# Kernel optimization log

Measured on AMD Instinct MI355X. Metric: run time of the kernel, lower is better.

The kernel has to match this reference:

```python
import jax, jax.numpy as jnp
import numpy as np

SQ3 = np.float32(np.sqrt(3.0))
NS, NV = 8, 4  # irreps 8x0e + 4x1o (dim 20)
N_NODES, N_EDGES = 10000, 160000


def _mlp(x, W1, W2):
    # e3nn FullyConnectedNet: act between layers, weights scaled by 1/sqrt(fan_in)
    h = jax.nn.relu(x @ (W1 / np.float32(np.sqrt(W1.shape[0]))))
    return h @ (W2 / np.float32(np.sqrt(W2.shape[0])))


def _tp(s, v, sh1, w_ss, w_vs, w_sv, w_vv):
    # FullyConnectedTensorProduct with per-edge weights, lmax=1 sh (sh0 == 1).
    # s:[E,Ms] scalars, v:[E,Mv,3] vectors, sh1:[E,3] component-normalized l=1 SH.
    Ms, Mv = s.shape[1], v.shape[1]
    c_s = np.float32(1.0 / np.sqrt(2.0 * Ms))
    c_v = np.float32(1.0 / np.sqrt(2.0 * Mv))
    # 0e x 0e -> 0e  and  1o x 1o -> 0e (dot / sqrt(3))
    dots = jnp.einsum('eic,ec->ei', v, sh1) / SQ3
    out0 = jnp.einsum('ei,eio->eo', s, w_ss) * c_s + jnp.einsum('ei,eio->eo', dots, w_vs) * c_v
    # 0e x 1o -> 1o  and  1o x 0e -> 1o
    out1 = jnp.einsum('ei,ec,eio->eoc', s, sh1, w_sv) * c_s + jnp.einsum('eic,eio->eoc', v, w_vv) * c_v
    return out0, out1


def setup_inputs() -> dict:
    key = jax.random.key(0)
    ks = jax.random.split(key, 16)
    N, E = N_NODES, N_EDGES
    return {
        'hn': jax.random.normal(ks[0], (N, 20), jnp.float32),
        'he': jax.random.normal(ks[1], (E, 20), jnp.float32),
        'edge_src': jax.random.randint(ks[2], (E,), 0, N),
        'edge_dst': jax.random.randint(ks[3], (E,), 0, N),
        'edge_vec': jax.random.normal(ks[4], (E, 3), jnp.float32),
        'emb': jax.random.uniform(ks[5], (E, 10), jnp.float32),
        'norm': jax.random.uniform(ks[6], (E,), jnp.float32),
        'num_nodes': N,
        'fcW1': jax.random.normal(ks[7], (10, 16), jnp.float32),
        'fcW2': jax.random.normal(ks[8], (16, 576), jnp.float32),
        'fc2W1': jax.random.normal(ks[9], (10, 16), jnp.float32),
        'fc2W2': jax.random.normal(ks[10], (16, 144), jnp.float32),
        'WgS': jax.random.normal(ks[11], (16, 12), jnp.float32),
        'WgV': jax.random.normal(ks[12], (8, 4), jnp.float32),
        'WoS': jax.random.normal(ks[13], (8, 8), jnp.float32),
        'WoV': jax.random.normal(ks[14], (4, 4), jnp.float32),
    }


def reference(hn, he, edge_src, edge_dst, edge_vec, emb, norm, num_nodes,
              fcW1, fcW2, fc2W1, fc2W2, WgS, WgV, WoS, WoV):
    E = he.shape[0]
    split = lambda x: (x[:, :NS], x[:, NS:].reshape(-1, NV, 3))
    hn_s, hn_v = split(hn)
    he_s, he_v = split(he)

    # spherical harmonics, normalize=True, component normalization, lmax=1
    sh1 = SQ3 * edge_vec / (jnp.linalg.norm(edge_vec, axis=1, keepdims=True) + 1e-12)

    s_in = jnp.concatenate([he_s, hn_s[edge_src], hn_s[edge_dst]], axis=1)       # [E,24]
    v_in = jnp.concatenate([he_v, hn_v[edge_src], hn_v[edge_dst]], axis=1)       # [E,12,3]

    # per-edge TP1 weights from tiny MLP on edge embedding (weight_numel = 576)
    w = _mlp(emb, fcW1, fcW2)
    w_ss = w[:, :288].reshape(E, 24, 12)
    w_vs = w[:, 288:432].reshape(E, 12, 12)
    w_sv = w[:, 432:528].reshape(E, 24, 4)
    w_vv = w[:, 528:576].reshape(E, 12, 4)
    g0, g1 = _tp(s_in, v_in, sh1, w_ss, w_vs, w_sv, w_vv)                        # [E,12],[E,4,3]

    # Gate: 8x0e scalars (ReLU), 4x0e gates (ReLU) gating 4x1o
    tmp_s = jax.nn.relu(g0[:, :NS])
    gates = jax.nn.relu(g0[:, NS:NS + NV])
    tmp_v = g1 * gates[:, :, None]

    # per-edge TP2 weights (weight_numel = 144)
    w2 = _mlp(emb, fc2W1, fc2W2)
    w2_ss = w2[:, :64].reshape(E, 8, 8)
    w2_vs = w2[:, 64:96].reshape(E, 4, 8)
    w2_sv = w2[:, 96:128].reshape(E, 8, 4)
    w2_vv = w2[:, 128:144].reshape(E, 4, 4)
    d0, d1 = _tp(tmp_s, tmp_v, sh1, w2_ss, w2_vs, w2_sv, w2_vv)

    he_new = jnp.concatenate([he_s + d0, (he_v + d1).reshape(E, NV * 3)], axis=1)

    # scatter-aggregate edge features to destination nodes
    node_ftr = jax.ops.segment_sum(he_new * norm[:, None], edge_dst, num_segments=num_nodes)
    nf_s, nf_v = node_ftr[:, :NS], node_ftr[:, NS:].reshape(-1, NV, 3)

    # lin = o3GatedLinear(input+output -> output) then o3.Linear(output -> output)
    cat_s = jnp.concatenate([hn_s, nf_s], axis=1)                                # [N,16]
    cat_v = jnp.concatenate([hn_v, nf_v], axis=1)                                # [N,8,3]
    g_lin = cat_s @ (WgS / np.float32(np.sqrt(16.0)))                            # [N,12]
    v_lin = jnp.einsum('nic,io->noc', cat_v, WgV) / np.float32(np.sqrt(8.0))     # [N,4,3]
    ls = jax.nn.relu(g_lin[:, :NS])
    lg = jax.nn.relu(g_lin[:, NS:])
    lv = v_lin * lg[:, :, None]
    out_s = ls @ (WoS / np.float32(np.sqrt(8.0)))
    out_v = jnp.einsum('nic,io->noc', lv, WoV) / np.float32(np.sqrt(4.0))

    hn_new = hn + jnp.concatenate([out_s, out_v.reshape(-1, NV * 3)], axis=1)
    return hn_new, he_new
```

## Files before the change

### kernel.cpp

```cpp
#include <hip/hip_runtime.h>

typedef __attribute__((ext_vector_type(8))) short bf16x8;
typedef __attribute__((ext_vector_type(4))) short bf16x4;
typedef __attribute__((ext_vector_type(4))) float f32x4;
typedef unsigned short ushort_t;

#define EPB 256
#define ST  32
#define W1S 632
#define W2S 168
#define HHS 40
#define TPS 40

__device__ __forceinline__ float frelu(float x) { return fmaxf(x, 0.0f); }

__device__ __forceinline__ ushort_t f2bf(float f) {
    unsigned u = __float_as_uint(f);
    u = (u + 0x7FFFu + ((u >> 16) & 1u)) >> 16;
    return (ushort_t)u;
}
__device__ __forceinline__ float bf2f(ushort_t u) {
    return __uint_as_float(((unsigned)u) << 16);
}

__device__ __forceinline__ float dot8(const float* s, bf16x8 w) {
    float a = 0.f;
#pragma unroll
    for (int b = 0; b < 8; ++b) a = fmaf(s[b], bf2f((ushort_t)w[b]), a);
    return a;
}
__device__ __forceinline__ float dot4(const float* s, bf16x4 w) {
    float a = 0.f;
#pragma unroll
    for (int b = 0; b < 4; ++b) a = fmaf(s[b], bf2f((ushort_t)w[b]), a);
    return a;
}

__global__ void prep_kernel(const float* __restrict__ fcW2,
                            const float* __restrict__ fc2W2,
                            ushort_t* __restrict__ W1t,
                            ushort_t* __restrict__ W2t) {
    const float SQ3 = 1.7320508075688772f;
    const float cs1 = 0.14433756729740643f;
    const float cv1 = 0.20412414523193150f;
    const float cs2 = 0.25f;
    const float cv2 = 0.35355339059327373f;
    int idx = blockIdx.x * blockDim.x + threadIdx.x;
    if (idx < 576 * 16) {
        int c = idx >> 4, k = idx & 15;
        float s = (c < 288) ? cs1 : (c < 432) ? cv1 : (c < 528) ? SQ3 * cs1 : cv1;
        W1t[idx] = f2bf(fcW2[k * 576 + c] * 0.25f * s);
    }
    if (idx < 144 * 16) {
        int c = idx >> 4, k = idx & 15;
        float s = (c < 64) ? cs2 : (c < 96) ? cv2 : (c < 128) ? SQ3 * cs2 : cv2;
        W2t[idx] = f2bf(fc2W2[k * 144 + c] * 0.25f * s);
    }
}

__global__ __launch_bounds__(EPB) void edge_kernel(
    const float* __restrict__ hn, const float* __restrict__ he,
    const int* __restrict__ esrc, const int* __restrict__ edst,
    const float* __restrict__ evec, const float* __restrict__ emb,
    const float* __restrict__ enorm,
    const float* __restrict__ fcW1, const float* __restrict__ fc2W1,
    const ushort_t* __restrict__ W1t, const ushort_t* __restrict__ W2t,
    float* __restrict__ he_out, float* __restrict__ node_ftr, int E) {

    __shared__ ushort_t hh[EPB][HHS];
    __shared__ ushort_t W1L[ST][W1S];
    __shared__ ushort_t W2L[ST][W2S];
    __shared__ ushort_t tmpL[ST][TPS];

    const int tid  = threadIdx.x;
    const int wave = tid >> 6;
    const int lane = tid & 63;
    const int row  = lane & 15;
    const int g    = lane >> 4;
    const long long blk = blockIdx.x;

    bf16x8 Bf[12];
#pragma unroll
    for (int idx = 0; idx < 12; ++idx) {
        int t = wave + idx * 4;
        bf16x8 v = {};
        if (t < 45 && g < 2) {
            const ushort_t* src = (t < 36) ? (W1t + (t * 16 + row) * 16 + g * 8)
                                           : (W2t + ((t - 36) * 16 + row) * 16 + g * 8);
            v = *reinterpret_cast<const bf16x8*>(src);
        }
        Bf[idx] = v;
    }

    {
        long long e0 = blk * EPB + tid;
        if (e0 < (long long)E) {
            float em[10];
#pragma unroll
            for (int i = 0; i < 10; ++i) em[i] = emb[e0 * 10 + i] * 0.31622776601683794f;
#pragma unroll
            for (int jj = 0; jj < 16; ++jj) {
                float a = 0.f, b = 0.f;
#pragma unroll
                for (int i = 0; i < 10; ++i) {
                    a = fmaf(em[i], fcW1[i * 16 + jj], a);
                    b = fmaf(em[i], fc2W1[i * 16 + jj], b);
                }
                hh[tid][jj]      = f2bf(frelu(a));
                hh[tid][16 + jj] = f2bf(frelu(b));
            }
        } else {
#pragma unroll
            for (int jj = 0; jj < 32; ++jj) hh[tid][jj] = 0;
        }
    }
    __syncthreads();

    const int le = tid & 31;
    const int j  = tid >> 5;

    for (int st = 0; st < 8; ++st) {
        long long ge = blk * EPB + st * ST + le;
        bool on = ge < (long long)E;

        int nd = 0;
        float ex = 0, ey = 0, ez = 0, nw = 0;
        float her[20], hsr[20], hdr[20];
        if (on) {
            int ns = esrc[ge];
            nd = edst[ge];
            ex = evec[ge * 3 + 0]; ey = evec[ge * 3 + 1]; ez = evec[ge * 3 + 2];
            nw = enorm[ge];
            const float* hp = he + ge * 20;
            const float* sp = hn + (long long)ns * 20;
            const float* dp = hn + (long long)nd * 20;
#pragma unroll
            for (int q = 0; q < 20; ++q) { her[q] = hp[q]; hsr[q] = sp[q]; hdr[q] = dp[q]; }
        } else {
#pragma unroll
            for (int q = 0; q < 20; ++q) { her[q] = 0; hsr[q] = 0; hdr[q] = 0; }
        }

        bf16x8 A1[2] = {}, A2[2] = {};
        if (g < 2) {
#pragma unroll
            for (int m = 0; m < 2; ++m) {
                A1[m] = *reinterpret_cast<const bf16x8*>(&hh[st * ST + m * 16 + row][g * 8]);
                A2[m] = *reinterpret_cast<const bf16x8*>(&hh[st * ST + m * 16 + row][16 + g * 8]);
            }
        }
#pragma unroll
        for (int idx = 0; idx < 12; ++idx) {
            int t = wave + idx * 4;
            if (t >= 45) continue;
            bool isg1 = (t < 36);
            int c = (isg1 ? t * 16 : (t - 36) * 16) + row;
            int off;
            if (isg1) {
                if (c < 288)      { int i = c / 12,          o = c % 12;         off = o * 24 + i; }
                else if (c < 432) { int i = (c - 288) / 12,  o = (c - 288) % 12; off = 288 + o * 12 + i; }
                else if (c < 528) { int i = (c - 432) >> 2,  o = (c - 432) & 3;  off = 432 + o * 24 + i; }
                else              { int i = (c - 528) >> 2,  o = (c - 528) & 3;  off = 528 + o * 12 + i; }
            } else {
                if (c < 64)       { int i = c >> 3,          o = c & 7;          off = o * 8 + i; }
                else if (c < 96)  { int i = (c - 64) >> 3,   o = (c - 64) & 7;   off = 64 + o * 4 + i; }
                else if (c < 128) { int i = (c - 96) >> 2,   o = (c - 96) & 3;   off = 96 + o * 8 + i; }
                else              { int i = (c - 128) >> 2,  o = (c - 128) & 3;  off = 128 + o * 4 + i; }
            }
            f32x4 zero = {0.f, 0.f, 0.f, 0.f};
#pragma unroll
            for (int m = 0; m < 2; ++m) {
                f32x4 d = __builtin_amdgcn_mfma_f32_16x16x32_bf16(isg1 ? A1[m] : A2[m], Bf[idx], zero, 0, 0, 0);
                int r0 = m * 16 + g * 4;
                if (isg1) {
#pragma unroll
                    for (int r = 0; r < 4; ++r) W1L[r0 + r][off] = f2bf(d[r]);
                } else {
#pragma unroll
                    for (int r = 0; r < 4; ++r) W2L[r0 + r][off] = f2bf(d[r]);
                }
            }
        }
        __syncthreads();

        float u0 = 0, u1 = 0, u2 = 0;
        if (on) {
            float inv = 1.0f / (sqrtf(fmaf(ex, ex, fmaf(ey, ey, ez * ez))) + 1e-12f);
            u0 = ex * inv; u1 = ey * inv; u2 = ez * inv;
            const ushort_t* base = &W1L[le][0];

            if (j < 6) {
                float dots[12];
#pragma unroll
                for (int i = 0; i < 4; ++i) {
                    dots[i]     = fmaf(her[8 + i * 3], u0, fmaf(her[9 + i * 3], u1, her[10 + i * 3] * u2));
                    dots[4 + i] = fmaf(hsr[8 + i * 3], u0, fmaf(hsr[9 + i * 3], u1, hsr[10 + i * 3] * u2));
                    dots[8 + i] = fmaf(hdr[8 + i * 3], u0, fmaf(hdr[9 + i * 3], u1, hdr[10 + i * 3] * u2));
                }
#pragma unroll
                for (int oo = 0; oo < 2; ++oo) {
                    int o = 2 * j + oo;
                    bf16x8 wa = *reinterpret_cast<const bf16x8*>(base + o * 24);
                    bf16x8 wb = *reinterpret_cast<const bf16x8*>(base + o * 24 + 8);
                    bf16x8 wc = *reinterpret_cast<const bf16x8*>(base + o * 24 + 16);
                    float acc = dot8(her, wa) + dot8(hsr, wb) + dot8(hdr, wc);
                    bf16x4 va = *reinterpret_cast<const bf16x4*>(base + 288 + o * 12);
                    bf16x4 vb = *reinterpret_cast<const bf16x4*>(base + 288 + o * 12 + 4);
                    bf16x4 vc = *reinterpret_cast<const bf16x4*>(base + 288 + o * 12 + 8);
                    acc += dot4(dots, va) + dot4(dots + 4, vb) + dot4(dots + 8, vc);
                    tmpL[le][o] = f2bf(acc);
                }
            } else {
#pragma unroll
                for (int oo = 0; oo < 2; ++oo) {
                    int o = 2 * (j - 6) + oo;
                    bf16x8 p0 = *reinterpret_cast<const bf16x8*>(base + 432 + o * 24);
                    bf16x8 p1 = *reinterpret_cast<const bf16x8*>(base + 432 + o * 24 + 8);
                    bf16x8 p2 = *reinterpret_cast<const bf16x8*>(base + 432 + o * 24 + 16);
                    float q = dot8(her, p0) + dot8(hsr, p1) + dot8(hdr, p2);
                    bf16x4 q0 = *reinterpret_cast<const bf16x4*>(base + 528 + o * 12);
                    bf16x4 q1 = *reinterpret_cast<const bf16x4*>(base + 528 + o * 12 + 4);
                    bf16x4 q2 = *reinterpret_cast<const bf16x4*>(base + 528 + o * 12 + 8);
                    float vx = 0, vy = 0, vz = 0;
#pragma unroll
                    for (int i = 0; i < 4; ++i) {
                        float w = bf2f((ushort_t)q0[i]);
                        vx = fmaf(her[8 + i * 3], w, vx); vy = fmaf(her[9 + i * 3], w, vy); vz = fmaf(her[10 + i * 3], w, vz);
                    }
#pragma unroll
                    for (int i = 0; i < 4; ++i) {
                        float w = bf2f((ushort_t)q1[i]);
                        vx = fmaf(hsr[8 + i * 3], w, vx); vy = fmaf(hsr[9 + i * 3], w, vy); vz = fmaf(hsr[10 + i * 3], w, vz);
                    }
#pragma unroll
                    for (int i = 0; i < 4; ++i) {
                        float w = bf2f((ushort_t)q2[i]);
                        vx = fmaf(hdr[8 + i * 3], w, vx); vy = fmaf(hdr[9 + i * 3], w, vy); vz = fmaf(hdr[10 + i * 3], w, vz);
                    }
                    tmpL[le][12 + 3 * o + 0] = f2bf(fmaf(q, u0, vx));
                    tmpL[le][12 + 3 * o + 1] = f2bf(fmaf(q, u1, vy));
                    tmpL[le][12 + 3 * o + 2] = f2bf(fmaf(q, u2, vz));
                }
            }
        }
        __syncthreads();

        if (on) {
            bf16x8 t0 = *reinterpret_cast<const bf16x8*>(&tmpL[le][0]);
            bf16x8 t1 = *reinterpret_cast<const bf16x8*>(&tmpL[le][8]);
            bf16x8 t2 = *reinterpret_cast<const bf16x8*>(&tmpL[le][16]);
            float ts[8];
#pragma unroll
            for (int b = 0; b < 8; ++b) ts[b] = frelu(bf2f((ushort_t)t0[b]));
            float gt[4];
#pragma unroll
            for (int o = 0; o < 4; ++o) gt[o] = frelu(bf2f((ushort_t)t1[o]));
            float tv[4][3];
#pragma unroll
            for (int o = 0; o < 4; ++o) {
#pragma unroll
                for (int c = 0; c < 3; ++c) {
                    int sl = 12 + 3 * o + c;
                    float raw = (sl < 16) ? bf2f((ushort_t)t1[sl - 8]) : bf2f((ushort_t)t2[sl - 16]);
                    tv[o][c] = raw * gt[o];
                }
            }
            float d2[4];
#pragma unroll
            for (int i = 0; i < 4; ++i) d2[i] = fmaf(tv[i][0], u0, fmaf(tv[i][1], u1, tv[i][2] * u2));

            const ushort_t* b2 = &W2L[le][0];
            float* hep = he_out + ge * 20;
            float* nf  = node_ftr + (long long)nd * 20;

            {
                bf16x8 wss = *reinterpret_cast<const bf16x8*>(b2 + j * 8);
                bf16x4 wvs = *reinterpret_cast<const bf16x4*>(b2 + 64 + j * 4);
                float dval = dot8(ts, wss) + dot4(d2, wvs);
                float oS = he[ge * 20 + j] + dval;
                hep[j] = oS;
                atomicAdd(nf + j, oS * nw);
            }
            if (j < 4) {
                bf16x8 wsv = *reinterpret_cast<const bf16x8*>(b2 + 96 + j * 8);
                float q2s = dot8(ts, wsv);
                bf16x4 wvv = *reinterpret_cast<const bf16x4*>(b2 + 128 + j * 4);
                float e0c = 0, e1c = 0, e2c = 0;
#pragma unroll
                for (int i = 0; i < 4; ++i) {
                    float w = bf2f((ushort_t)wvv[i]);
                    e0c = fmaf(tv[i][0], w, e0c); e1c = fmaf(tv[i][1], w, e1c); e2c = fmaf(tv[i][2], w, e2c);
                }
                float d1c[3] = { fmaf(q2s, u0, e0c), fmaf(q2s, u1, e1c), fmaf(q2s, u2, e2c) };
#pragma unroll
                for (int c = 0; c < 3; ++c) {
                    float oV = he[ge * 20 + 8 + 3 * j + c] + d1c[c];
                    hep[8 + 3 * j + c] = oV;
                    atomicAdd(nf + 8 + 3 * j + c, oV * nw);
                }
            }
        }
        __syncthreads();
    }
}

__global__ __launch_bounds__(256) void node_kernel(
    const float* __restrict__ hn, const float* __restrict__ node_ftr,
    const float* __restrict__ WgS, const float* __restrict__ WgV,
    const float* __restrict__ WoS, const float* __restrict__ WoV,
    float* __restrict__ out, int N) {
    int n = blockIdx.x * blockDim.x + threadIdx.x;
    if (n >= N) return;
    const float* hr = hn + (size_t)n * 20;
    const float* fr = node_ftr + (size_t)n * 20;
    const float rs16 = 0.25f, rs8 = 0.35355339059327373f, rs4 = 0.5f;

    float cs[16], cvx[8], cvy[8], cvz[8];
#pragma unroll
    for (int i = 0; i < 8; ++i) { cs[i] = hr[i]; cs[8 + i] = fr[i]; }
#pragma unroll
    for (int i = 0; i < 4; ++i) {
        cvx[i] = hr[8 + i * 3]; cvy[i] = hr[8 + i * 3 + 1]; cvz[i] = hr[8 + i * 3 + 2];
        cvx[4 + i] = fr[8 + i * 3]; cvy[4 + i] = fr[8 + i * 3 + 1]; cvz[4 + i] = fr[8 + i * 3 + 2];
    }
    float gl[12];
#pragma unroll
    for (int o = 0; o < 12; ++o) {
        float a = 0.f;
#pragma unroll
        for (int i = 0; i < 16; ++i) a = fmaf(cs[i], WgS[i * 12 + o], a);
        gl[o] = a * rs16;
    }
    float vlx[4], vly[4], vlz[4];
#pragma unroll
    for (int o = 0; o < 4; ++o) {
        float ax = 0.f, ay = 0.f, az = 0.f;
#pragma unroll
        for (int i = 0; i < 8; ++i) {
            float w = WgV[i * 4 + o];
            ax = fmaf(cvx[i], w, ax); ay = fmaf(cvy[i], w, ay); az = fmaf(cvz[i], w, az);
        }
        float gv = frelu(gl[8 + o]);
        vlx[o] = ax * rs8 * gv; vly[o] = ay * rs8 * gv; vlz[o] = az * rs8 * gv;
    }
    float ls[8];
#pragma unroll
    for (int i = 0; i < 8; ++i) ls[i] = frelu(gl[i]);
    float* op = out + (size_t)n * 20;
#pragma unroll
    for (int o = 0; o < 8; ++o) {
        float a = 0.f;
#pragma unroll
        for (int i = 0; i < 8; ++i) a = fmaf(ls[i], WoS[i * 8 + o], a);
        op[o] = hr[o] + a * rs8;
    }
#pragma unroll
    for (int o = 0; o < 4; ++o) {
        float ax = 0.f, ay = 0.f, az = 0.f;
#pragma unroll
        for (int i = 0; i < 4; ++i) {
            float w = WoV[i * 4 + o];
            ax = fmaf(vlx[i], w, ax); ay = fmaf(vly[i], w, ay); az = fmaf(vlz[i], w, az);
        }
        op[8 + o * 3 + 0] = hr[8 + o * 3 + 0] + ax * rs4;
        op[8 + o * 3 + 1] = hr[8 + o * 3 + 1] + ay * rs4;
        op[8 + o * 3 + 2] = hr[8 + o * 3 + 2] + az * rs4;
    }
}

extern "C" void kernel_launch(void* const* d_in, const int* in_sizes, int n_in,
                              void* d_out, int out_size, void* d_ws, size_t ws_size,
                              hipStream_t stream) {
    const float* hn    = (const float*)d_in[0];
    const float* he    = (const float*)d_in[1];
    const int*   esrc  = (const int*)d_in[2];
    const int*   edst  = (const int*)d_in[3];
    const float* evec  = (const float*)d_in[4];
    const float* emb   = (const float*)d_in[5];
    const float* enorm = (const float*)d_in[6];
    const float* fcW1  = (const float*)d_in[8];
    const float* fcW2  = (const float*)d_in[9];
    const float* fc2W1 = (const float*)d_in[10];
    const float* fc2W2 = (const float*)d_in[11];
    const float* WgS   = (const float*)d_in[12];
    const float* WgV   = (const float*)d_in[13];
    const float* WoS   = (const float*)d_in[14];
    const float* WoV   = (const float*)d_in[15];

    int N = in_sizes[0] / 20;
    int E = in_sizes[1] / 20;

    float* out      = (float*)d_out;
    float* he_out   = out + (size_t)N * 20;
    float* node_ftr = (float*)d_ws;
    ushort_t* W1t   = (ushort_t*)(node_ftr + (size_t)N * 20);
    ushort_t* W2t   = W1t + 576 * 16;

    hipMemsetAsync(node_ftr, 0, (size_t)N * 20 * sizeof(float), stream);
    prep_kernel<<<(576 * 16 + 255) / 256, 256, 0, stream>>>(fcW2, fc2W2, W1t, W2t);
    edge_kernel<<<(E + EPB - 1) / EPB, EPB, 0, stream>>>(
        hn, he, esrc, edst, evec, emb, enorm, fcW1, fc2W1, W1t, W2t, he_out, node_ftr, E);
    node_kernel<<<(N + 255) / 256, 256, 0, stream>>>(hn, node_ftr, WgS, WgV, WoS, WoV, out, N);
}
```

Baseline: 256.2 us.

## Halve edge sub-tile and spread per-edge outputs across more threads

Shrinks the per-iteration sub-tile from 32 to 16 edges, so each of the 256 threads computes one output channel instead of two, and the final stage splits scalar and vector outputs across separate thread groups. The goal is to cut serial work per thread and the shared weight tile footprint. In exchange there are twice as many loop iterations and block barriers, and each MFMA call covers half as many rows, so weight generation may use the matrix unit less efficiently. The node-feature memset is also folded into the prep kernel to drop one launch.

```diff
diff --git a/kernel.cpp b/kernel.cpp
--- a/kernel.cpp
+++ b/kernel.cpp
@@ -6,7 +6,7 @@
 typedef unsigned short ushort_t;
 
 #define EPB 256
-#define ST  32
+#define ST  16
 #define W1S 632
 #define W2S 168
 #define HHS 40
@@ -39,7 +39,8 @@
 __global__ void prep_kernel(const float* __restrict__ fcW2,
                             const float* __restrict__ fc2W2,
                             ushort_t* __restrict__ W1t,
-                            ushort_t* __restrict__ W2t) {
+                            ushort_t* __restrict__ W2t,
+                            float* __restrict__ node_ftr, int nfcount) {
     const float SQ3 = 1.7320508075688772f;
     const float cs1 = 0.14433756729740643f;
     const float cv1 = 0.20412414523193150f;
@@ -56,6 +57,7 @@
         float s = (c < 64) ? cs2 : (c < 96) ? cv2 : (c < 128) ? SQ3 * cs2 : cv2;
         W2t[idx] = f2bf(fc2W2[k * 144 + c] * 0.25f * s);
     }
+    if (idx < nfcount) node_ftr[idx] = 0.f;
 }
 
 __global__ __launch_bounds__(EPB) void edge_kernel(
@@ -116,10 +118,10 @@
     }
     __syncthreads();
 
-    const int le = tid & 31;
-    const int j  = tid >> 5;
-
-    for (int st = 0; st < 8; ++st) {
+    const int le = tid & 15;
+    const int j  = tid >> 4;
+
+    for (int st = 0; st < 16; ++st) {
         long long ge = blk * EPB + st * ST + le;
         bool on = ge < (long long)E;
 
@@ -141,13 +143,10 @@
             for (int q = 0; q < 20; ++q) { her[q] = 0; hsr[q] = 0; hdr[q] = 0; }
         }
 
-        bf16x8 A1[2] = {}, A2[2] = {};
+        bf16x8 A1 = {}, A2 = {};
         if (g < 2) {
-#pragma unroll
-            for (int m = 0; m < 2; ++m) {
-                A1[m] = *reinterpret_cast<const bf16x8*>(&hh[st * ST + m * 16 + row][g * 8]);
-                A2[m] = *reinterpret_cast<const bf16x8*>(&hh[st * ST + m * 16 + row][16 + g * 8]);
-            }
+            A1 = *reinterpret_cast<const bf16x8*>(&hh[st * ST + row][g * 8]);
+            A2 = *reinterpret_cast<const bf16x8*>(&hh[st * ST + row][16 + g * 8]);
         }
 #pragma unroll
         for (int idx = 0; idx < 12; ++idx) {
@@ -168,17 +167,14 @@
                 else              { int i = (c - 128) >> 2,  o = (c - 128) & 3;  off = 128 + o * 4 + i; }
             }
             f32x4 zero = {0.f, 0.f, 0.f, 0.f};
-#pragma unroll
-            for (int m = 0; m < 2; ++m) {
-                f32x4 d = __builtin_amdgcn_mfma_f32_16x16x32_bf16(isg1 ? A1[m] : A2[m], Bf[idx], zero, 0, 0, 0);
-                int r0 = m * 16 + g * 4;
-                if (isg1) {
-#pragma unroll
-                    for (int r = 0; r < 4; ++r) W1L[r0 + r][off] = f2bf(d[r]);
-                } else {
-#pragma unroll
-                    for (int r = 0; r < 4; ++r) W2L[r0 + r][off] = f2bf(d[r]);
-                }
+            f32x4 d = __builtin_amdgcn_mfma_f32_16x16x32_bf16(isg1 ? A1 : A2, Bf[idx], zero, 0, 0, 0);
+            int r0 = g * 4;
+            if (isg1) {
+#pragma unroll
+                for (int r = 0; r < 4; ++r) W1L[r0 + r][off] = f2bf(d[r]);
+            } else {
+#pragma unroll
+                for (int r = 0; r < 4; ++r) W2L[r0 + r][off] = f2bf(d[r]);
             }
         }
         __syncthreads();
@@ -189,7 +185,7 @@
             u0 = ex * inv; u1 = ey * inv; u2 = ez * inv;
             const ushort_t* base = &W1L[le][0];
 
-            if (j < 6) {
+            if (j < 12) {
                 float dots[12];
 #pragma unroll
                 for (int i = 0; i < 4; ++i) {
@@ -197,55 +193,49 @@
                     dots[4 + i] = fmaf(hsr[8 + i * 3], u0, fmaf(hsr[9 + i * 3], u1, hsr[10 + i * 3] * u2));
                     dots[8 + i] = fmaf(hdr[8 + i * 3], u0, fmaf(hdr[9 + i * 3], u1, hdr[10 + i * 3] * u2));
                 }
-#pragma unroll
-                for (int oo = 0; oo < 2; ++oo) {
-                    int o = 2 * j + oo;
-                    bf16x8 wa = *reinterpret_cast<const bf16x8*>(base + o * 24);
-                    bf16x8 wb = *reinterpret_cast<const bf16x8*>(base + o * 24 + 8);
-                    bf16x8 wc = *reinterpret_cast<const bf16x8*>(base + o * 24 + 16);
-                    float acc = dot8(her, wa) + dot8(hsr, wb) + dot8(hdr, wc);
-                    bf16x4 va = *reinterpret_cast<const bf16x4*>(base + 288 + o * 12);
-                    bf16x4 vb = *reinterpret_cast<const bf16x4*>(base + 288 + o * 12 + 4);
-                    bf16x4 vc = *reinterpret_cast<const bf16x4*>(base + 288 + o * 12 + 8);
-                    acc += dot4(dots, va) + dot4(dots + 4, vb) + dot4(dots + 8, vc);
-                    tmpL[le][o] = f2bf(acc);
-                }
+                int o = j;
+                bf16x8 wa = *reinterpret_cast<const bf16x8*>(base + o * 24);
+                bf16x8 wb = *reinterpret_cast<const bf16x8*>(base + o * 24 + 8);
+                bf16x8 wc = *reinterpret_cast<const bf16x8*>(base + o * 24 + 16);
+                float acc = dot8(her, wa) + dot8(hsr, wb) + dot8(hdr, wc);
+                bf16x4 va = *reinterpret_cast<const bf16x4*>(base + 288 + o * 12);
+                bf16x4 vb = *reinterpret_cast<const bf16x4*>(base + 288 + o * 12 + 4);
+                bf16x4 vc = *reinterpret_cast<const bf16x4*>(base + 288 + o * 12 + 8);
+                acc += dot4(dots, va) + dot4(dots + 4, vb) + dot4(dots + 8, vc);
+                tmpL[le][o] = f2bf(acc);
             } else {
-#pragma unroll
-                for (int oo = 0; oo < 2; ++oo) {
-                    int o = 2 * (j - 6) + oo;
-                    bf16x8 p0 = *reinterpret_cast<const bf16x8*>(base + 432 + o * 24);
-                    bf16x8 p1 = *reinterpret_cast<const bf16x8*>(base + 432 + o * 24 + 8);
-                    bf16x8 p2 = *reinterpret_cast<const bf16x8*>(base + 432 + o * 24 + 16);
-                    float q = dot8(her, p0) + dot8(hsr, p1) + dot8(hdr, p2);
-                    bf16x4 q0 = *reinterpret_cast<const bf16x4*>(base + 528 + o * 12);
-                    bf16x4 q1 = *reinterpret_cast<const bf16x4*>(base + 528 + o * 12 + 4);
-                    bf16x4 q2 = *reinterpret_cast<const bf16x4*>(base + 528 + o * 12 + 8);
-                    float vx = 0, vy = 0, vz = 0;
-#pragma unroll
-                    for (int i = 0; i < 4; ++i) {
-                        float w = bf2f((ushort_t)q0[i]);
-                        vx = fmaf(her[8 + i * 3], w, vx); vy = fmaf(her[9 + i * 3], w, vy); vz = fmaf(her[10 + i * 3], w, vz);
-                    }
-#pragma unroll
-                    for (int i = 0; i < 4; ++i) {
-                        float w = bf2f((ushort_t)q1[i]);
-                        vx = fmaf(hsr[8 + i * 3], w, vx); vy = fmaf(hsr[9 + i * 3], w, vy); vz = fmaf(hsr[10 + i * 3], w, vz);
-                    }
-#pragma unroll
-                    for (int i = 0; i < 4; ++i) {
-                        float w = bf2f((ushort_t)q2[i]);
-                        vx = fmaf(hdr[8 + i * 3], w, vx); vy = fmaf(hdr[9 + i * 3], w, vy); vz = fmaf(hdr[10 + i * 3], w, vz);
-                    }
-                    tmpL[le][12 + 3 * o + 0] = f2bf(fmaf(q, u0, vx));
-                    tmpL[le][12 + 3 * o + 1] = f2bf(fmaf(q, u1, vy));
-                    tmpL[le][12 + 3 * o + 2] = f2bf(fmaf(q, u2, vz));
-                }
+                int o = j - 12;
+                bf16x8 p0 = *reinterpret_cast<const bf16x8*>(base + 432 + o * 24);
+                bf16x8 p1 = *reinterpret_cast<const bf16x8*>(base + 432 + o * 24 + 8);
+                bf16x8 p2 = *reinterpret_cast<const bf16x8*>(base + 432 + o * 24 + 16);
+                float q = dot8(her, p0) + dot8(hsr, p1) + dot8(hdr, p2);
+                bf16x4 q0 = *reinterpret_cast<const bf16x4*>(base + 528 + o * 12);
+                bf16x4 q1 = *reinterpret_cast<const bf16x4*>(base + 528 + o * 12 + 4);
+                bf16x4 q2 = *reinterpret_cast<const bf16x4*>(base + 528 + o * 12 + 8);
+                float vx = 0, vy = 0, vz = 0;
+#pragma unroll
+                for (int i = 0; i < 4; ++i) {
+                    float w = bf2f((ushort_t)q0[i]);
+                    vx = fmaf(her[8 + i * 3], w, vx); vy = fmaf(her[9 + i * 3], w, vy); vz = fmaf(her[10 + i * 3], w, vz);
+                }
+#pragma unroll
+                for (int i = 0; i < 4; ++i) {
+                    float w = bf2f((ushort_t)q1[i]);
+                    vx = fmaf(hsr[8 + i * 3], w, vx); vy = fmaf(hsr[9 + i * 3], w, vy); vz = fmaf(hsr[10 + i * 3], w, vz);
+                }
+#pragma unroll
+                for (int i = 0; i < 4; ++i) {
+                    float w = bf2f((ushort_t)q2[i]);
+                    vx = fmaf(hdr[8 + i * 3], w, vx); vy = fmaf(hdr[9 + i * 3], w, vy); vz = fmaf(hdr[10 + i * 3], w, vz);
+                }
+                tmpL[le][12 + 3 * o + 0] = f2bf(fmaf(q, u0, vx));
+                tmpL[le][12 + 3 * o + 1] = f2bf(fmaf(q, u1, vy));
+                tmpL[le][12 + 3 * o + 2] = f2bf(fmaf(q, u2, vz));
             }
         }
         __syncthreads();
 
-        if (on) {
+        if (on && j < 12) {
             bf16x8 t0 = *reinterpret_cast<const bf16x8*>(&tmpL[le][0]);
             bf16x8 t1 = *reinterpret_cast<const bf16x8*>(&tmpL[le][8]);
             bf16x8 t2 = *reinterpret_cast<const bf16x8*>(&tmpL[le][16]);
@@ -273,18 +263,18 @@
             float* hep = he_out + ge * 20;
             float* nf  = node_ftr + (long long)nd * 20;
 
-            {
+            if (j < 8) {
                 bf16x8 wss = *reinterpret_cast<const bf16x8*>(b2 + j * 8);
                 bf16x4 wvs = *reinterpret_cast<const bf16x4*>(b2 + 64 + j * 4);
                 float dval = dot8(ts, wss) + dot4(d2, wvs);
                 float oS = he[ge * 20 + j] + dval;
                 hep[j] = oS;
                 atomicAdd(nf + j, oS * nw);
-            }
-            if (j < 4) {
-                bf16x8 wsv = *reinterpret_cast<const bf16x8*>(b2 + 96 + j * 8);
+            } else {
+                int o = j - 8;
+                bf16x8 wsv = *reinterpret_cast<const bf16x8*>(b2 + 96 + o * 8);
                 float q2s = dot8(ts, wsv);
-                bf16x4 wvv = *reinterpret_cast<const bf16x4*>(b2 + 128 + j * 4);
+                bf16x4 wvv = *reinterpret_cast<const bf16x4*>(b2 + 128 + o * 4);
                 float e0c = 0, e1c = 0, e2c = 0;
 #pragma unroll
                 for (int i = 0; i < 4; ++i) {
@@ -294,9 +284,9 @@
                 float d1c[3] = { fmaf(q2s, u0, e0c), fmaf(q2s, u1, e1c), fmaf(q2s, u2, e2c) };
 #pragma unroll
                 for (int c = 0; c < 3; ++c) {
-                    float oV = he[ge * 20 + 8 + 3 * j + c] + d1c[c];
-                    hep[8 + 3 * j + c] = oV;
-                    atomicAdd(nf + 8 + 3 * j + c, oV * nw);
+                    float oV = he[ge * 20 + 8 + 3 * o + c] + d1c[c];
+                    hep[8 + 3 * o + c] = oV;
+                    atomicAdd(nf + 8 + 3 * o + c, oV * nw);
                 }
             }
         }
@@ -396,8 +386,9 @@
     ushort_t* W1t   = (ushort_t*)(node_ftr + (size_t)N * 20);
     ushort_t* W2t   = W1t + 576 * 16;
 
-    hipMemsetAsync(node_ftr, 0, (size_t)N * 20 * sizeof(float), stream);
-    prep_kernel<<<(576 * 16 + 255) / 256, 256, 0, stream>>>(fcW2, fc2W2, W1t, W2t);
+    int nfcount = N * 20;
+    int prep_work = (nfcount > 576 * 16) ? nfcount : 576 * 16;
+    prep_kernel<<<(prep_work + 255) / 256, 256, 0, stream>>>(fcW2, fc2W2, W1t, W2t, node_ftr, nfcount);
     edge_kernel<<<(E + EPB - 1) / EPB, EPB, 0, stream>>>(
         hn, he, esrc, edst, evec, emb, enorm, fcW1, fc2W1, W1t, W2t, he_out, node_ftr, E);
     node_kernel<<<(N + 255) / 256, 256, 0, stream>>>(hn, node_ftr, WgS, WgV, WoS, WoV, out, N);
```

Result: faster. 211.4 us (-17.5%).
